# Kernel optimization log

Hardware: AMD Instinct MI355X
Metric: run time of the kernel (lower is better)

Reference implementation:

```python
import jax, jax.numpy as jnp
import numpy as np

B, T, CH, Hs, Ws = 2, 64, 512, 24, 24
DIM = CH // 2          # 256, attention channel dim
HEADS = 8
HEAD_DIM = DIM // HEADS  # 32
MAX_SEQ = 64


def setup_inputs() -> dict:
    key = jax.random.key(0)
    ks = jax.random.split(key, 6)
    return {
        "x": jax.random.normal(ks[0], (B, T, CH, Hs, Ws), dtype=jnp.float32),
        "rpb_table": jax.random.normal(ks[1], (2 * MAX_SEQ - 1, HEADS), dtype=jnp.float32) * 0.02,
        "qkv_w": jax.random.normal(ks[2], (3 * DIM, DIM), dtype=jnp.float32) * 0.02,
        "qkv_b": jax.random.normal(ks[3], (3 * DIM,), dtype=jnp.float32) * 0.02,
        "proj_w": jax.random.normal(ks[4], (DIM, DIM), dtype=jnp.float32) * 0.02,
        "proj_b": jax.random.normal(ks[5], (DIM,), dtype=jnp.float32) * 0.02,
    }


def reference(x, rpb_table, qkv_w, qkv_b, proj_w, proj_b):
    b, t, c, h, w = x.shape
    half = c // 2
    a_part = x[:, :, :half]       # (B,T,half,H,W) untouched branch
    b_part = x[:, :, half:]       # attention branch

    # 'b t c h w -> (b h w) t c'
    xb = jnp.transpose(b_part, (0, 3, 4, 1, 2)).reshape(b * h * w, t, half)
    B_, N, C = xb.shape
    scale = HEAD_DIM ** -0.5

    qkv = xb @ qkv_w.T + qkv_b                        # (B_, N, 3*C)
    qkv = qkv.reshape(B_, N, 3, HEADS, HEAD_DIM)
    qkv = jnp.transpose(qkv, (2, 0, 3, 1, 4))          # (3, B_, heads, N, hd)
    q, k, v = qkv[0] * scale, qkv[1], qkv[2]

    attn = jnp.einsum('bhnd,bhmd->bhnm', q, k)         # (B_, heads, N, N)

    # relative position bias: index = p2 - p1 + (MAX_SEQ - 1)
    pos = jnp.arange(t)
    rel_idx = pos[None, :] - pos[:, None] + (MAX_SEQ - 1)   # (N, N)
    bias = rpb_table[rel_idx]                              # (N, N, heads)
    bias = jnp.transpose(bias, (2, 0, 1))                  # (heads, N, N)
    attn = attn + bias[None]

    # causal (mask_future=True): -inf strictly above the diagonal
    causal = jnp.where(pos[None, :] > pos[:, None], -jnp.inf, 0.0).astype(attn.dtype)
    attn = attn + causal[None, None]

    attn = jax.nn.softmax(attn, axis=-1)

    out = jnp.einsum('bhnm,bhmd->bhnd', attn, v)       # (B_, heads, N, hd)
    out = jnp.transpose(out, (0, 2, 1, 3)).reshape(B_, N, C)
    out = out @ proj_w.T + proj_b

    # '(b h w) t c -> b t c h w'
    out = out.reshape(b, h, w, t, half)
    out = jnp.transpose(out, (0, 3, 4, 1, 2))

    return jnp.concatenate([a_part, out], axis=2)
```

## Files before the change

kernel.cpp:

```cpp
#include <hip/hip_runtime.h>
#include <hip/hip_bf16.h>

typedef __attribute__((ext_vector_type(4))) float  f32x4;
typedef __attribute__((ext_vector_type(8))) short  bf16x8;
typedef __attribute__((ext_vector_type(8))) unsigned short u16x8;
typedef __attribute__((ext_vector_type(4))) unsigned short u16x4;
typedef __attribute__((ext_vector_type(4))) int i32x4;

__device__ __forceinline__ unsigned short f2bf(float f) {
    union { float f; unsigned u; } v; v.f = f;
    unsigned u = v.u;
    unsigned r = u + 0x7fffu + ((u >> 16) & 1u);
    return (unsigned short)(r >> 16);
}

__device__ __forceinline__ unsigned cvtpk(float lo, float hi) {
    unsigned r;
    asm("v_cvt_pk_bf16_f32 %0, %1, %2" : "=v"(r) : "v"(lo), "v"(hi));
    return r;
}

__device__ __forceinline__ int selshfl(unsigned lo, unsigned hiw, int srcLane, bool hi) {
    int a = __shfl((int)lo, srcLane, 64);
    int b = __shfl((int)hiw, srcLane, 64);
    return hi ? b : a;
}

__device__ __forceinline__ bf16x8 mkfrag(int w0, int w1, int w2, int w3) {
    i32x4 t; t[0] = w0; t[1] = w1; t[2] = w2; t[3] = w3;
    return __builtin_bit_cast(bf16x8, t);
}

__device__ __forceinline__ void gload16(const void* g, void* l) {
    __builtin_amdgcn_global_load_lds((const __attribute__((address_space(1))) unsigned*)g,
                                     (__attribute__((address_space(3))) unsigned*)l, 16, 0, 0);
}

#define MFMA(A, B, C) __builtin_amdgcn_mfma_f32_16x16x32_bf16((A), (B), (C), 0, 0, 0)


__global__ void cvt_weights(const float* __restrict__ qkv_w, const float* __restrict__ proj_w,
                            unsigned short* __restrict__ wq, unsigned short* __restrict__ wp) {
    int i = blockIdx.x * 256 + threadIdx.x;
    if (i < 196608) wq[i] = f2bf(qkv_w[i]);
    else            wp[i - 196608] = f2bf(proj_w[i - 196608]);
}

__global__ __launch_bounds__(256) void transpose_b(const float* __restrict__ x,
                                                   unsigned short* __restrict__ xb,
                                                   float* __restrict__ outp) {
    __shared__ unsigned short tile[256][72];
    const int bt  = blockIdx.x;
    const int hw0 = blockIdx.y * 64;
    const int tid = threadIdx.x;
    {
        const size_t slab = (size_t)bt * 294912;
        #pragma unroll
        for (int it = 0; it < 16; ++it) {
            int idx = it * 256 + tid;
            int ch  = idx >> 4;
            int off = (idx & 15) * 4;
            size_t o = slab + (size_t)ch * 576 + hw0 + off;
            *(float4*)(outp + o) = *(const float4*)(x + o);
        }
    }
    const float* src = x + ((size_t)bt * 512 + 256) * 576 + hw0;
    const int c_sub = tid >> 4, l16 = tid & 15;
    #pragma unroll
    for (int it = 0; it < 16; ++it) {
        int cc = it * 16 + c_sub;
        const float4 v = *(const float4*)(src + (size_t)cc * 576 + l16 * 4);
        tile[cc][l16 * 4 + 0] = f2bf(v.x);
        tile[cc][l16 * 4 + 1] = f2bf(v.y);
        tile[cc][l16 * 4 + 2] = f2bf(v.z);
        tile[cc][l16 * 4 + 3] = f2bf(v.w);
    }
    __syncthreads();
    const int row = tid >> 2;
    const int cs  = (tid & 3) * 64;
    const int b = bt >> 6, t = bt & 63;
    size_t m = ((size_t)(b * 576 + hw0 + row)) * 64 + t;
    unsigned short* dst = xb + m * 256 + cs;
    #pragma unroll
    for (int q = 0; q < 8; ++q) {
        u16x8 v;
        #pragma unroll
        for (int u = 0; u < 8; ++u) v[u] = tile[cs + q * 8 + u][row];
        *(u16x8*)(dst + q * 8) = v;
    }
}

#define PKPAIR(D, A, B4) \
    const unsigned D##_0 = cvtpk(A[0] + B4.x, A[1] + B4.y); \
    const unsigned D##_1 = cvtpk(A[2] + B4.z, A[3] + B4.w);

#define MKF(DST, LO, HI_) \
    DST = mkfrag(selshfl(LO##_0, HI_##_0, lA, hi), selshfl(LO##_1, HI_##_1, lA, hi), \
                 selshfl(LO##_0, HI_##_0, lB, hi), selshfl(LO##_1, HI_##_1, lB, hi));

#define SM1(SC, JT, R) { \
    const int j_ = (JT) * 16 + 4 * g + (R); \
    int d_ = j_ - i_ + 63; d_ = d_ > 63 ? 63 : d_; \
    const float v_ = SC[R] * scale + bias_w[d_]; \
    const float e_ = (j_ > i_) ? 0.f : __expf(v_); \
    SC[R] = e_; rs += e_; }

#define SMROW(SC, JT) SM1(SC, JT, 0) SM1(SC, JT, 1) SM1(SC, JT, 2) SM1(SC, JT, 3)

#define ATT_COL(IT, QF, O0V, O1V) { \
    f32x4 Sc0{0.f,0.f,0.f,0.f}, Sc1{0.f,0.f,0.f,0.f}, Sc2{0.f,0.f,0.f,0.f}, Sc3{0.f,0.f,0.f,0.f}; \
    __builtin_amdgcn_s_setprio(1); \
    Sc0 = MFMA(kf0, QF, Sc0); Sc1 = MFMA(kf1, QF, Sc1); \
    Sc2 = MFMA(kf2, QF, Sc2); Sc3 = MFMA(kf3, QF, Sc3); \
    __builtin_amdgcn_s_setprio(0); \
    const int i_ = (IT) * 16 + c; \
    float rs = 0.f; \
    SMROW(Sc0, 0) SMROW(Sc1, 1) SMROW(Sc2, 2) SMROW(Sc3, 3) \
    rs += __shfl_xor(rs, 16, 64); \
    rs += __shfl_xor(rs, 32, 64); \
    const float inv = 1.0f / rs; \
    const unsigned p00 = cvtpk(Sc0[0]*inv, Sc0[1]*inv), p01 = cvtpk(Sc0[2]*inv, Sc0[3]*inv); \
    const unsigned p10 = cvtpk(Sc1[0]*inv, Sc1[1]*inv), p11 = cvtpk(Sc1[2]*inv, Sc1[3]*inv); \
    const unsigned p20 = cvtpk(Sc2[0]*inv, Sc2[1]*inv), p21 = cvtpk(Sc2[2]*inv, Sc2[3]*inv); \
    const unsigned p30 = cvtpk(Sc3[0]*inv, Sc3[1]*inv), p31 = cvtpk(Sc3[2]*inv, Sc3[3]*inv); \
    const bf16x8 pf0 = mkfrag(selshfl(p00, p10, lA, hi), selshfl(p01, p11, lA, hi), \
                              selshfl(p00, p10, lB, hi), selshfl(p01, p11, lB, hi)); \
    const bf16x8 pf1 = mkfrag(selshfl(p20, p30, lA, hi), selshfl(p21, p31, lA, hi), \
                              selshfl(p20, p30, lB, hi), selshfl(p21, p31, lB, hi)); \
    __builtin_amdgcn_s_setprio(1); \
    O0V = MFMA(vf00, pf0, O0V); O1V = MFMA(vf10, pf0, O1V); \
    O0V = MFMA(vf01, pf1, O0V); O1V = MFMA(vf11, pf1, O1V); \
    __builtin_amdgcn_s_setprio(0); }

#define OSTORE(OV, DT, IT) { \
    const int t_ = (IT) * 16 + c; \
    const int unit_ = w * 4 + (DT) * 2 + (g >> 1); \
    u16x4 v_; v_[0] = f2bf(OV[0]); v_[1] = f2bf(OV[1]); v_[2] = f2bf(OV[2]); v_[3] = f2bf(OV[3]); \
    *(u16x4*)(&xs[t_ * 256 + ((unit_ ^ (t_ & 7)) << 3) + 4 * (g & 1)]) = v_; }

__global__ __launch_bounds__(512, 4)
void fused_block(
    const unsigned short* __restrict__ xb,
    const unsigned short* __restrict__ wqkv,
    const unsigned short* __restrict__ wproj,
    const float* __restrict__ qkv_b,
    const float* __restrict__ proj_b,
    const float* __restrict__ rpb,
    float* __restrict__ out)
{
    __shared__ unsigned short xs[16384];
    __shared__ unsigned short VtAll[256 * 88];
    __shared__ float bias_s[8][64];

    const int tid  = threadIdx.x;
    const int lane = tid & 63, w = tid >> 6;
    const int c = lane & 15, g = lane >> 4;
    const int c7 = c & 7;
    const bool hi = g >= 2;
    const int lA = c + 16 * ((2 * g) & 3);
    const int lB = c + 16 * ((2 * g + 1) & 3);
    const int bid = blockIdx.x;
    const int p  = (bid & 7) * 144 + (bid >> 3);
    const int b  = p / 576, hw = p % 576;

    const unsigned short* src = xb + (size_t)p * 16384;
    #pragma unroll
    for (int it = 0; it < 4; ++it) {
        int U = it * 512 + tid;
        int r = U >> 5, u = U & 31;
        gload16(src + r * 256 + ((u ^ (r & 7)) << 3), &xs[U << 3]);
    }
    bias_s[tid & 7][tid >> 3] = rpb[tid];
    __syncthreads();

    const float* bias_w = bias_s[w];
    const float scale = 0.17677669529663687f;

    {
        f32x4 acc[2][4] = {};
        #pragma unroll
        for (int ks = 0; ks < 8; ++ks) {
            bf16x8 bx[4], af[2];
            #pragma unroll
            for (int b2 = 0; b2 < 4; ++b2)
                bx[b2] = *(const bf16x8*)(&xs[(b2 * 16 + c) * 256 + (((ks * 4 + g) ^ c7) << 3)]);
            #pragma unroll
            for (int a2 = 0; a2 < 2; ++a2)
                af[a2] = *(const bf16x8*)(wqkv + (size_t)(512 + w * 32 + a2 * 16 + c) * 256 + ks * 32 + g * 8);
            #pragma unroll
            for (int a2 = 0; a2 < 2; ++a2)
                #pragma unroll
                for (int b2 = 0; b2 < 4; ++b2)
                    acc[a2][b2] = MFMA(af[a2], bx[b2], acc[a2][b2]);
        }
        #pragma unroll
        for (int a2 = 0; a2 < 2; ++a2) {
            float4 bv = *(const float4*)(qkv_b + 512 + w * 32 + a2 * 16 + g * 4);
            #pragma unroll
            for (int b2 = 0; b2 < 4; ++b2) {
                int t = b2 * 16 + c;
                VtAll[(w * 32 + a2 * 16 + g * 4 + 0) * 88 + t] = f2bf(acc[a2][b2][0] + bv.x);
                VtAll[(w * 32 + a2 * 16 + g * 4 + 1) * 88 + t] = f2bf(acc[a2][b2][1] + bv.y);
                VtAll[(w * 32 + a2 * 16 + g * 4 + 2) * 88 + t] = f2bf(acc[a2][b2][2] + bv.z);
                VtAll[(w * 32 + a2 * 16 + g * 4 + 3) * 88 + t] = f2bf(acc[a2][b2][3] + bv.w);
            }
        }
    }

    bf16x8 kf0, kf1, kf2, kf3, qf0, qf1, qf2, qf3;
    {
        f32x4 ak[2][4] = {}, aq[2][4] = {};
        #pragma unroll
        for (int ks = 0; ks < 8; ++ks) {
            bf16x8 bx[4], afk[2], afq[2];
            #pragma unroll
            for (int b2 = 0; b2 < 4; ++b2)
                bx[b2] = *(const bf16x8*)(&xs[(b2 * 16 + c) * 256 + (((ks * 4 + g) ^ c7) << 3)]);
            #pragma unroll
            for (int a2 = 0; a2 < 2; ++a2) {
                afk[a2] = *(const bf16x8*)(wqkv + (size_t)(256 + w * 32 + a2 * 16 + c) * 256 + ks * 32 + g * 8);
                afq[a2] = *(const bf16x8*)(wqkv + (size_t)(      w * 32 + a2 * 16 + c) * 256 + ks * 32 + g * 8);
            }
            #pragma unroll
            for (int a2 = 0; a2 < 2; ++a2)
                #pragma unroll
                for (int b2 = 0; b2 < 4; ++b2) {
                    ak[a2][b2] = MFMA(afk[a2], bx[b2], ak[a2][b2]);
                    aq[a2][b2] = MFMA(afq[a2], bx[b2], aq[a2][b2]);
                }
        }
        const float4 bk0 = *(const float4*)(qkv_b + 256 + w * 32 + g * 4);
        const float4 bk1 = *(const float4*)(qkv_b + 256 + w * 32 + 16 + g * 4);
        const float4 bq0 = *(const float4*)(qkv_b +       w * 32 + g * 4);
        const float4 bq1 = *(const float4*)(qkv_b +       w * 32 + 16 + g * 4);
        PKPAIR(kp00, ak[0][0], bk0) PKPAIR(kp01, ak[0][1], bk0)
        PKPAIR(kp02, ak[0][2], bk0) PKPAIR(kp03, ak[0][3], bk0)
        PKPAIR(kp10, ak[1][0], bk1) PKPAIR(kp11, ak[1][1], bk1)
        PKPAIR(kp12, ak[1][2], bk1) PKPAIR(kp13, ak[1][3], bk1)
        PKPAIR(qp00, aq[0][0], bq0) PKPAIR(qp01, aq[0][1], bq0)
        PKPAIR(qp02, aq[0][2], bq0) PKPAIR(qp03, aq[0][3], bq0)
        PKPAIR(qp10, aq[1][0], bq1) PKPAIR(qp11, aq[1][1], bq1)
        PKPAIR(qp12, aq[1][2], bq1) PKPAIR(qp13, aq[1][3], bq1)
        MKF(kf0, kp00, kp10) MKF(kf1, kp01, kp11) MKF(kf2, kp02, kp12) MKF(kf3, kp03, kp13)
        MKF(qf0, qp00, qp10) MKF(qf1, qp01, qp11) MKF(qf2, qp02, qp12) MKF(qf3, qp03, qp13)
    }

    const bf16x8 vf00 = *(const bf16x8*)(&VtAll[(w * 32 +  0 + c) * 88 +  0 + g * 8]);
    const bf16x8 vf01 = *(const bf16x8*)(&VtAll[(w * 32 +  0 + c) * 88 + 32 + g * 8]);
    const bf16x8 vf10 = *(const bf16x8*)(&VtAll[(w * 32 + 16 + c) * 88 +  0 + g * 8]);
    const bf16x8 vf11 = *(const bf16x8*)(&VtAll[(w * 32 + 16 + c) * 88 + 32 + g * 8]);

    f32x4 O00{0.f,0.f,0.f,0.f}, O01{0.f,0.f,0.f,0.f}, O02{0.f,0.f,0.f,0.f}, O03{0.f,0.f,0.f,0.f};
    f32x4 O10{0.f,0.f,0.f,0.f}, O11{0.f,0.f,0.f,0.f}, O12{0.f,0.f,0.f,0.f}, O13{0.f,0.f,0.f,0.f};
    ATT_COL(0, qf0, O00, O10)
    ATT_COL(1, qf1, O01, O11)
    ATT_COL(2, qf2, O02, O12)
    ATT_COL(3, qf3, O03, O13)

    __syncthreads();
    OSTORE(O00, 0, 0) OSTORE(O01, 0, 1) OSTORE(O02, 0, 2) OSTORE(O03, 0, 3)
    OSTORE(O10, 1, 0) OSTORE(O11, 1, 1) OSTORE(O12, 1, 2) OSTORE(O13, 1, 3)
    __syncthreads();

    f32x4 ap[2][4] = {};
    #pragma unroll
    for (int ks = 0; ks < 8; ++ks) {
        bf16x8 af[2], bx[4];
        #pragma unroll
        for (int a2 = 0; a2 < 2; ++a2)
            af[a2] = *(const bf16x8*)(wproj + (size_t)(w * 32 + a2 * 16 + c) * 256 + ks * 32 + g * 8);
        #pragma unroll
        for (int b2 = 0; b2 < 4; ++b2)
            bx[b2] = *(const bf16x8*)(&xs[(b2 * 16 + c) * 256 + (((ks * 4 + g) ^ c7) << 3)]);
        #pragma unroll
        for (int a2 = 0; a2 < 2; ++a2)
            #pragma unroll
            for (int b2 = 0; b2 < 4; ++b2)
                ap[a2][b2] = MFMA(af[a2], bx[b2], ap[a2][b2]);
    }
    #pragma unroll
    for (int a2 = 0; a2 < 2; ++a2) {
        int n = w * 32 + a2 * 16 + g * 4;
        float4 pb = *(const float4*)(proj_b + n);
        #pragma unroll
        for (int b2 = 0; b2 < 4; ++b2) {
            int t = b2 * 16 + c;
            float* dst = out + ((size_t)((b * 64 + t) * 512 + 256 + n)) * 576 + hw;
            dst[0]        = ap[a2][b2][0] + pb.x;
            dst[576]      = ap[a2][b2][1] + pb.y;
            dst[2 * 576]  = ap[a2][b2][2] + pb.z;
            dst[3 * 576]  = ap[a2][b2][3] + pb.w;
        }
    }
}

extern "C" void kernel_launch(void* const* d_in, const int* in_sizes, int n_in,
                              void* d_out, int out_size, void* d_ws, size_t ws_size,
                              hipStream_t stream) {
    (void)in_sizes; (void)n_in; (void)out_size;
    const float* x      = (const float*)d_in[0];
    const float* rpb    = (const float*)d_in[1];
    const float* qkv_w  = (const float*)d_in[2];
    const float* qkv_b  = (const float*)d_in[3];
    const float* proj_w = (const float*)d_in[4];
    const float* proj_b = (const float*)d_in[5];
    float* out = (float*)d_out;

    char* ws = (char*)d_ws;
    unsigned short* wq = (unsigned short*)ws;
    unsigned short* wp = (unsigned short*)(ws + 393216);
    unsigned short* xb = (unsigned short*)(ws + 524288);
    if (ws_size < (size_t)524288 + 37748736) return;

    cvt_weights<<<1024, 256, 0, stream>>>(qkv_w, proj_w, wq, wp);
    transpose_b<<<dim3(128, 9), 256, 0, stream>>>(x, xb, out);
    fused_block<<<1152, 512, 0, stream>>>(xb, wq, wp, qkv_b, proj_b, rpb, out);
}
```

Measured before the change: 247.4 us.

## Split fused block into per-head attention kernel plus separate tiled projection GEMM

Replaces the single fused kernel, which handled one spatial position with 512 threads, with two kernels. The first is a per-head attention kernel with one wave per (position, head): it computes Q, K and V by reading x directly from global memory, then writes the bf16 attention output to a new workspace buffer. The second is a separate 128x128 tiled GEMM for the output projection, with LDS staging and swizzling. The aim is to raise occupancy and parallelism and to make the projection GEMM more efficient. The cost is an extra round trip through global memory for the intermediate of about 37MB, plus an additional kernel launch; the setprio hints are also removed.

```diff
diff --git a/kernel.cpp b/kernel.cpp
--- a/kernel.cpp
+++ b/kernel.cpp
@@ -109,10 +109,8 @@
 
 #define ATT_COL(IT, QF, O0V, O1V) { \
     f32x4 Sc0{0.f,0.f,0.f,0.f}, Sc1{0.f,0.f,0.f,0.f}, Sc2{0.f,0.f,0.f,0.f}, Sc3{0.f,0.f,0.f,0.f}; \
-    __builtin_amdgcn_s_setprio(1); \
     Sc0 = MFMA(kf0, QF, Sc0); Sc1 = MFMA(kf1, QF, Sc1); \
     Sc2 = MFMA(kf2, QF, Sc2); Sc3 = MFMA(kf3, QF, Sc3); \
-    __builtin_amdgcn_s_setprio(0); \
     const int i_ = (IT) * 16 + c; \
     float rs = 0.f; \
     SMROW(Sc0, 0) SMROW(Sc1, 1) SMROW(Sc2, 2) SMROW(Sc3, 3) \
@@ -127,112 +125,85 @@
                               selshfl(p00, p10, lB, hi), selshfl(p01, p11, lB, hi)); \
     const bf16x8 pf1 = mkfrag(selshfl(p20, p30, lA, hi), selshfl(p21, p31, lA, hi), \
                               selshfl(p20, p30, lB, hi), selshfl(p21, p31, lB, hi)); \
-    __builtin_amdgcn_s_setprio(1); \
     O0V = MFMA(vf00, pf0, O0V); O1V = MFMA(vf10, pf0, O1V); \
-    O0V = MFMA(vf01, pf1, O0V); O1V = MFMA(vf11, pf1, O1V); \
-    __builtin_amdgcn_s_setprio(0); }
-
-#define OSTORE(OV, DT, IT) { \
+    O0V = MFMA(vf01, pf1, O0V); O1V = MFMA(vf11, pf1, O1V); }
+
+#define OSTOREG(OV, DT, IT) { \
     const int t_ = (IT) * 16 + c; \
-    const int unit_ = w * 4 + (DT) * 2 + (g >> 1); \
     u16x4 v_; v_[0] = f2bf(OV[0]); v_[1] = f2bf(OV[1]); v_[2] = f2bf(OV[2]); v_[3] = f2bf(OV[3]); \
-    *(u16x4*)(&xs[t_ * 256 + ((unit_ ^ (t_ & 7)) << 3) + 4 * (g & 1)]) = v_; }
-
-__global__ __launch_bounds__(512, 4)
-void fused_block(
+    *(u16x4*)(att + ((size_t)(t_ * 1152 + p)) * 256 + h * 32 + (DT) * 16 + 4 * g) = v_; }
+
+__global__ __launch_bounds__(256, 3)
+void attn_heads(
     const unsigned short* __restrict__ xb,
     const unsigned short* __restrict__ wqkv,
-    const unsigned short* __restrict__ wproj,
     const float* __restrict__ qkv_b,
-    const float* __restrict__ proj_b,
     const float* __restrict__ rpb,
-    float* __restrict__ out)
+    unsigned short* __restrict__ att)
 {
-    __shared__ unsigned short xs[16384];
-    __shared__ unsigned short VtAll[256 * 88];
+    __shared__ unsigned short vt[4][32 * 88];
     __shared__ float bias_s[8][64];
 
     const int tid  = threadIdx.x;
     const int lane = tid & 63, w = tid >> 6;
     const int c = lane & 15, g = lane >> 4;
-    const int c7 = c & 7;
     const bool hi = g >= 2;
     const int lA = c + 16 * ((2 * g) & 3);
     const int lB = c + 16 * ((2 * g + 1) & 3);
-    const int bid = blockIdx.x;
-    const int p  = (bid & 7) * 144 + (bid >> 3);
-    const int b  = p / 576, hw = p % 576;
-
-    const unsigned short* src = xb + (size_t)p * 16384;
-    #pragma unroll
-    for (int it = 0; it < 4; ++it) {
-        int U = it * 512 + tid;
-        int r = U >> 5, u = U & 31;
-        gload16(src + r * 256 + ((u ^ (r & 7)) << 3), &xs[U << 3]);
-    }
+
     bias_s[tid & 7][tid >> 3] = rpb[tid];
+    bias_s[(tid + 256) & 7][(tid + 256) >> 3] = rpb[tid + 256];
     __syncthreads();
 
-    const float* bias_w = bias_s[w];
+    const int gw = blockIdx.x * 4 + w;
+    const int h  = gw / 1152;
+    const int p  = gw - h * 1152;
+    const float* bias_w = bias_s[h];
     const float scale = 0.17677669529663687f;
-
-    {
-        f32x4 acc[2][4] = {};
-        #pragma unroll
-        for (int ks = 0; ks < 8; ++ks) {
-            bf16x8 bx[4], af[2];
-            #pragma unroll
-            for (int b2 = 0; b2 < 4; ++b2)
-                bx[b2] = *(const bf16x8*)(&xs[(b2 * 16 + c) * 256 + (((ks * 4 + g) ^ c7) << 3)]);
-            #pragma unroll
-            for (int a2 = 0; a2 < 2; ++a2)
-                af[a2] = *(const bf16x8*)(wqkv + (size_t)(512 + w * 32 + a2 * 16 + c) * 256 + ks * 32 + g * 8);
-            #pragma unroll
-            for (int a2 = 0; a2 < 2; ++a2)
-                #pragma unroll
-                for (int b2 = 0; b2 < 4; ++b2)
-                    acc[a2][b2] = MFMA(af[a2], bx[b2], acc[a2][b2]);
-        }
+    const unsigned short* xrow = xb + (size_t)p * 16384;
+    unsigned short* vts = vt[w];
+
+    f32x4 aq[2][4] = {}, ak[2][4] = {}, av[2][4] = {};
+    #pragma unroll
+    for (int ks = 0; ks < 8; ++ks) {
+        bf16x8 bx[4];
+        #pragma unroll
+        for (int b2 = 0; b2 < 4; ++b2)
+            bx[b2] = *(const bf16x8*)(xrow + (b2 * 16 + c) * 256 + ks * 32 + g * 8);
         #pragma unroll
         for (int a2 = 0; a2 < 2; ++a2) {
-            float4 bv = *(const float4*)(qkv_b + 512 + w * 32 + a2 * 16 + g * 4);
+            const size_t ko = (size_t)ks * 32 + g * 8;
+            const bf16x8 fq = *(const bf16x8*)(wqkv + (size_t)(      h * 32 + a2 * 16 + c) * 256 + ko);
+            const bf16x8 fk = *(const bf16x8*)(wqkv + (size_t)(256 + h * 32 + a2 * 16 + c) * 256 + ko);
+            const bf16x8 fv = *(const bf16x8*)(wqkv + (size_t)(512 + h * 32 + a2 * 16 + c) * 256 + ko);
             #pragma unroll
             for (int b2 = 0; b2 < 4; ++b2) {
-                int t = b2 * 16 + c;
-                VtAll[(w * 32 + a2 * 16 + g * 4 + 0) * 88 + t] = f2bf(acc[a2][b2][0] + bv.x);
-                VtAll[(w * 32 + a2 * 16 + g * 4 + 1) * 88 + t] = f2bf(acc[a2][b2][1] + bv.y);
-                VtAll[(w * 32 + a2 * 16 + g * 4 + 2) * 88 + t] = f2bf(acc[a2][b2][2] + bv.z);
-                VtAll[(w * 32 + a2 * 16 + g * 4 + 3) * 88 + t] = f2bf(acc[a2][b2][3] + bv.w);
+                aq[a2][b2] = MFMA(fq, bx[b2], aq[a2][b2]);
+                ak[a2][b2] = MFMA(fk, bx[b2], ak[a2][b2]);
+                av[a2][b2] = MFMA(fv, bx[b2], av[a2][b2]);
             }
+        }
+    }
+
+    #pragma unroll
+    for (int a2 = 0; a2 < 2; ++a2) {
+        float4 bv = *(const float4*)(qkv_b + 512 + h * 32 + a2 * 16 + g * 4);
+        #pragma unroll
+        for (int b2 = 0; b2 < 4; ++b2) {
+            int t = b2 * 16 + c;
+            vts[(a2 * 16 + g * 4 + 0) * 88 + t] = f2bf(av[a2][b2][0] + bv.x);
+            vts[(a2 * 16 + g * 4 + 1) * 88 + t] = f2bf(av[a2][b2][1] + bv.y);
+            vts[(a2 * 16 + g * 4 + 2) * 88 + t] = f2bf(av[a2][b2][2] + bv.z);
+            vts[(a2 * 16 + g * 4 + 3) * 88 + t] = f2bf(av[a2][b2][3] + bv.w);
         }
     }
 
     bf16x8 kf0, kf1, kf2, kf3, qf0, qf1, qf2, qf3;
     {
-        f32x4 ak[2][4] = {}, aq[2][4] = {};
-        #pragma unroll
-        for (int ks = 0; ks < 8; ++ks) {
-            bf16x8 bx[4], afk[2], afq[2];
-            #pragma unroll
-            for (int b2 = 0; b2 < 4; ++b2)
-                bx[b2] = *(const bf16x8*)(&xs[(b2 * 16 + c) * 256 + (((ks * 4 + g) ^ c7) << 3)]);
-            #pragma unroll
-            for (int a2 = 0; a2 < 2; ++a2) {
-                afk[a2] = *(const bf16x8*)(wqkv + (size_t)(256 + w * 32 + a2 * 16 + c) * 256 + ks * 32 + g * 8);
-                afq[a2] = *(const bf16x8*)(wqkv + (size_t)(      w * 32 + a2 * 16 + c) * 256 + ks * 32 + g * 8);
-            }
-            #pragma unroll
-            for (int a2 = 0; a2 < 2; ++a2)
-                #pragma unroll
-                for (int b2 = 0; b2 < 4; ++b2) {
-                    ak[a2][b2] = MFMA(afk[a2], bx[b2], ak[a2][b2]);
-                    aq[a2][b2] = MFMA(afq[a2], bx[b2], aq[a2][b2]);
-                }
-        }
-        const float4 bk0 = *(const float4*)(qkv_b + 256 + w * 32 + g * 4);
-        const float4 bk1 = *(const float4*)(qkv_b + 256 + w * 32 + 16 + g * 4);
-        const float4 bq0 = *(const float4*)(qkv_b +       w * 32 + g * 4);
-        const float4 bq1 = *(const float4*)(qkv_b +       w * 32 + 16 + g * 4);
+        const float4 bk0 = *(const float4*)(qkv_b + 256 + h * 32 + g * 4);
+        const float4 bk1 = *(const float4*)(qkv_b + 256 + h * 32 + 16 + g * 4);
+        const float4 bq0 = *(const float4*)(qkv_b +       h * 32 + g * 4);
+        const float4 bq1 = *(const float4*)(qkv_b +       h * 32 + 16 + g * 4);
         PKPAIR(kp00, ak[0][0], bk0) PKPAIR(kp01, ak[0][1], bk0)
         PKPAIR(kp02, ak[0][2], bk0) PKPAIR(kp03, ak[0][3], bk0)
         PKPAIR(kp10, ak[1][0], bk1) PKPAIR(kp11, ak[1][1], bk1)
@@ -245,10 +216,10 @@
         MKF(qf0, qp00, qp10) MKF(qf1, qp01, qp11) MKF(qf2, qp02, qp12) MKF(qf3, qp03, qp13)
     }
 
-    const bf16x8 vf00 = *(const bf16x8*)(&VtAll[(w * 32 +  0 + c) * 88 +  0 + g * 8]);
-    const bf16x8 vf01 = *(const bf16x8*)(&VtAll[(w * 32 +  0 + c) * 88 + 32 + g * 8]);
-    const bf16x8 vf10 = *(const bf16x8*)(&VtAll[(w * 32 + 16 + c) * 88 +  0 + g * 8]);
-    const bf16x8 vf11 = *(const bf16x8*)(&VtAll[(w * 32 + 16 + c) * 88 + 32 + g * 8]);
+    const bf16x8 vf00 = *(const bf16x8*)(&vts[( 0 + c) * 88 +  0 + g * 8]);
+    const bf16x8 vf01 = *(const bf16x8*)(&vts[( 0 + c) * 88 + 32 + g * 8]);
+    const bf16x8 vf10 = *(const bf16x8*)(&vts[(16 + c) * 88 +  0 + g * 8]);
+    const bf16x8 vf11 = *(const bf16x8*)(&vts[(16 + c) * 88 + 32 + g * 8]);
 
     f32x4 O00{0.f,0.f,0.f,0.f}, O01{0.f,0.f,0.f,0.f}, O02{0.f,0.f,0.f,0.f}, O03{0.f,0.f,0.f,0.f};
     f32x4 O10{0.f,0.f,0.f,0.f}, O11{0.f,0.f,0.f,0.f}, O12{0.f,0.f,0.f,0.f}, O13{0.f,0.f,0.f,0.f};
@@ -257,39 +228,66 @@
     ATT_COL(2, qf2, O02, O12)
     ATT_COL(3, qf3, O03, O13)
 
-    __syncthreads();
-    OSTORE(O00, 0, 0) OSTORE(O01, 0, 1) OSTORE(O02, 0, 2) OSTORE(O03, 0, 3)
-    OSTORE(O10, 1, 0) OSTORE(O11, 1, 1) OSTORE(O12, 1, 2) OSTORE(O13, 1, 3)
-    __syncthreads();
-
-    f32x4 ap[2][4] = {};
-    #pragma unroll
-    for (int ks = 0; ks < 8; ++ks) {
-        bf16x8 af[2], bx[4];
-        #pragma unroll
-        for (int a2 = 0; a2 < 2; ++a2)
-            af[a2] = *(const bf16x8*)(wproj + (size_t)(w * 32 + a2 * 16 + c) * 256 + ks * 32 + g * 8);
-        #pragma unroll
-        for (int b2 = 0; b2 < 4; ++b2)
-            bx[b2] = *(const bf16x8*)(&xs[(b2 * 16 + c) * 256 + (((ks * 4 + g) ^ c7) << 3)]);
-        #pragma unroll
-        for (int a2 = 0; a2 < 2; ++a2)
+    OSTOREG(O00, 0, 0) OSTOREG(O01, 0, 1) OSTOREG(O02, 0, 2) OSTOREG(O03, 0, 3)
+    OSTOREG(O10, 1, 0) OSTOREG(O11, 1, 1) OSTOREG(O12, 1, 2) OSTOREG(O13, 1, 3)
+}
+
+__global__ __launch_bounds__(256, 4) void gemm_proj(const unsigned short* __restrict__ A,
+                                                    const unsigned short* __restrict__ Wt,
+                                                    const float* __restrict__ bias,
+                                                    float* __restrict__ out) {
+    __shared__ unsigned short Ws[128 * 64];
+    __shared__ unsigned short Xs[128 * 64];
+    const int m0 = blockIdx.x * 128, n0 = blockIdx.y * 128;
+    const int tid = threadIdx.x;
+    const int lane = tid & 63, w = tid >> 6;
+    const int wy = w >> 1, wx = w & 1;
+    const int c = lane & 15, g = lane >> 4;
+    const int lr = lane >> 3, lu = lane & 7;
+    const int su = lu ^ lr;
+    const int cs7 = c & 7;
+    f32x4 acc[4][4] = {};
+    for (int k0 = 0; k0 < 256; k0 += 64) {
+        #pragma unroll
+        for (int q = 0; q < 4; ++q) {
+            int R = w * 32 + q * 8;
+            gload16(Wt + (size_t)(n0 + R + lr) * 256 + k0 + su * 8, &Ws[R * 64]);
+            gload16(A  + (size_t)(m0 + R + lr) * 256 + k0 + su * 8, &Xs[R * 64]);
+        }
+        __syncthreads();
+        #pragma unroll
+        for (int kk = 0; kk < 2; ++kk) {
+            bf16x8 af[4], bx[4];
+            #pragma unroll
+            for (int a2 = 0; a2 < 4; ++a2)
+                af[a2] = *(const bf16x8*)(&Ws[(wy * 64 + a2 * 16 + c) * 64 + (((kk * 4 + g) ^ cs7) * 8)]);
             #pragma unroll
             for (int b2 = 0; b2 < 4; ++b2)
-                ap[a2][b2] = MFMA(af[a2], bx[b2], ap[a2][b2]);
-    }
-    #pragma unroll
-    for (int a2 = 0; a2 < 2; ++a2) {
-        int n = w * 32 + a2 * 16 + g * 4;
-        float4 pb = *(const float4*)(proj_b + n);
+                bx[b2] = *(const bf16x8*)(&Xs[(wx * 64 + b2 * 16 + c) * 64 + (((kk * 4 + g) ^ cs7) * 8)]);
+            #pragma unroll
+            for (int a2 = 0; a2 < 4; ++a2)
+                #pragma unroll
+                for (int b2 = 0; b2 < 4; ++b2)
+                    acc[a2][b2] = MFMA(af[a2], bx[b2], acc[a2][b2]);
+        }
+        __syncthreads();
+    }
+    #pragma unroll
+    for (int a2 = 0; a2 < 4; ++a2) {
+        int n = n0 + wy * 64 + a2 * 16 + g * 4;
+        float4 bv = *(const float4*)(bias + n);
         #pragma unroll
         for (int b2 = 0; b2 < 4; ++b2) {
-            int t = b2 * 16 + c;
-            float* dst = out + ((size_t)((b * 64 + t) * 512 + 256 + n)) * 576 + hw;
-            dst[0]        = ap[a2][b2][0] + pb.x;
-            dst[576]      = ap[a2][b2][1] + pb.y;
-            dst[2 * 576]  = ap[a2][b2][2] + pb.z;
-            dst[3 * 576]  = ap[a2][b2][3] + pb.w;
+            int m = m0 + wx * 64 + b2 * 16 + c;
+            int t   = m / 1152;
+            int rem = m % 1152;
+            int bb  = rem / 576;
+            int hw  = rem % 576;
+            float* dst = out + ((size_t)(bb * 64 + t) * 512 + 256 + n) * 576 + hw;
+            dst[0]        = acc[a2][b2][0] + bv.x;
+            dst[576]      = acc[a2][b2][1] + bv.y;
+            dst[2 * 576]  = acc[a2][b2][2] + bv.z;
+            dst[3 * 576]  = acc[a2][b2][3] + bv.w;
         }
     }
 }
@@ -307,12 +305,14 @@
     float* out = (float*)d_out;
 
     char* ws = (char*)d_ws;
-    unsigned short* wq = (unsigned short*)ws;
-    unsigned short* wp = (unsigned short*)(ws + 393216);
-    unsigned short* xb = (unsigned short*)(ws + 524288);
-    if (ws_size < (size_t)524288 + 37748736) return;
+    unsigned short* wq  = (unsigned short*)ws;
+    unsigned short* wp  = (unsigned short*)(ws + 393216);
+    unsigned short* xb  = (unsigned short*)(ws + 524288);
+    unsigned short* att = (unsigned short*)(ws + 524288 + 37748736);
+    if (ws_size < (size_t)524288 + 2 * 37748736) return;
 
     cvt_weights<<<1024, 256, 0, stream>>>(qkv_w, proj_w, wq, wp);
     transpose_b<<<dim3(128, 9), 256, 0, stream>>>(x, xb, out);
-    fused_block<<<1152, 512, 0, stream>>>(xb, wq, wp, qkv_b, proj_b, rpb, out);
-}
+    attn_heads<<<2304, 256, 0, stream>>>(xb, wq, qkv_b, rpb, att);
+    gemm_proj<<<dim3(576, 2), 256, 0, stream>>>(att, wp, proj_b, out);
+}
```

Result: faster. 227.5 us (-8.1%).

## Read activations directly from global and merge QKV GEMMs into one pass

Applied to the files above, without the earlier changes.

The x tile is no longer staged into LDS with global_load_lds. Each wave reads its B fragments straight from global memory, and the Q, K and V projections are computed in a single k-loop that reuses each activation fragment across three weight sets. V^T and the attention output now share one smaller LDS region, which lowers LDS use per block and should allow more occupancy. The setprio hints around the MFMAs are removed. Every wave now reloads the same 32 KB activation tile from global or L2, which replaces cheap LDS reads with uncoalesced global reads. The fused loop also holds more accumulators live, raising register pressure.

```diff
diff --git a/kernel.cpp b/kernel.cpp
--- a/kernel.cpp
+++ b/kernel.cpp
@@ -29,11 +29,6 @@
 __device__ __forceinline__ bf16x8 mkfrag(int w0, int w1, int w2, int w3) {
     i32x4 t; t[0] = w0; t[1] = w1; t[2] = w2; t[3] = w3;
     return __builtin_bit_cast(bf16x8, t);
-}
-
-__device__ __forceinline__ void gload16(const void* g, void* l) {
-    __builtin_amdgcn_global_load_lds((const __attribute__((address_space(1))) unsigned*)g,
-                                     (__attribute__((address_space(3))) unsigned*)l, 16, 0, 0);
 }
 
 #define MFMA(A, B, C) __builtin_amdgcn_mfma_f32_16x16x32_bf16((A), (B), (C), 0, 0, 0)
@@ -109,10 +104,8 @@
 
 #define ATT_COL(IT, QF, O0V, O1V) { \
     f32x4 Sc0{0.f,0.f,0.f,0.f}, Sc1{0.f,0.f,0.f,0.f}, Sc2{0.f,0.f,0.f,0.f}, Sc3{0.f,0.f,0.f,0.f}; \
-    __builtin_amdgcn_s_setprio(1); \
     Sc0 = MFMA(kf0, QF, Sc0); Sc1 = MFMA(kf1, QF, Sc1); \
     Sc2 = MFMA(kf2, QF, Sc2); Sc3 = MFMA(kf3, QF, Sc3); \
-    __builtin_amdgcn_s_setprio(0); \
     const int i_ = (IT) * 16 + c; \
     float rs = 0.f; \
     SMROW(Sc0, 0) SMROW(Sc1, 1) SMROW(Sc2, 2) SMROW(Sc3, 3) \
@@ -127,19 +120,17 @@
                               selshfl(p00, p10, lB, hi), selshfl(p01, p11, lB, hi)); \
     const bf16x8 pf1 = mkfrag(selshfl(p20, p30, lA, hi), selshfl(p21, p31, lA, hi), \
                               selshfl(p20, p30, lB, hi), selshfl(p21, p31, lB, hi)); \
-    __builtin_amdgcn_s_setprio(1); \
     O0V = MFMA(vf00, pf0, O0V); O1V = MFMA(vf10, pf0, O1V); \
-    O0V = MFMA(vf01, pf1, O0V); O1V = MFMA(vf11, pf1, O1V); \
-    __builtin_amdgcn_s_setprio(0); }
+    O0V = MFMA(vf01, pf1, O0V); O1V = MFMA(vf11, pf1, O1V); }
 
 #define OSTORE(OV, DT, IT) { \
     const int t_ = (IT) * 16 + c; \
     const int unit_ = w * 4 + (DT) * 2 + (g >> 1); \
     u16x4 v_; v_[0] = f2bf(OV[0]); v_[1] = f2bf(OV[1]); v_[2] = f2bf(OV[2]); v_[3] = f2bf(OV[3]); \
-    *(u16x4*)(&xs[t_ * 256 + ((unit_ ^ (t_ & 7)) << 3) + 4 * (g & 1)]) = v_; }
+    *(u16x4*)(&att_s[t_ * 256 + ((unit_ ^ (t_ & 7)) << 3) + 4 * (g & 1)]) = v_; }
 
 __global__ __launch_bounds__(512, 4)
-void fused_block(
+void fused_attn_proj(
     const unsigned short* __restrict__ xb,
     const unsigned short* __restrict__ wqkv,
     const unsigned short* __restrict__ wproj,
@@ -148,8 +139,7 @@
     const float* __restrict__ rpb,
     float* __restrict__ out)
 {
-    __shared__ unsigned short xs[16384];
-    __shared__ unsigned short VtAll[256 * 88];
+    __shared__ unsigned short region[18432];
     __shared__ float bias_s[8][64];
 
     const int tid  = threadIdx.x;
@@ -159,80 +149,61 @@
     const bool hi = g >= 2;
     const int lA = c + 16 * ((2 * g) & 3);
     const int lB = c + 16 * ((2 * g + 1) & 3);
+
+    bias_s[tid & 7][tid >> 3] = rpb[tid];
+    __syncthreads();
+
+    const int h  = w;
     const int bid = blockIdx.x;
     const int p  = (bid & 7) * 144 + (bid >> 3);
     const int b  = p / 576, hw = p % 576;
-
-    const unsigned short* src = xb + (size_t)p * 16384;
-    #pragma unroll
-    for (int it = 0; it < 4; ++it) {
-        int U = it * 512 + tid;
-        int r = U >> 5, u = U & 31;
-        gload16(src + r * 256 + ((u ^ (r & 7)) << 3), &xs[U << 3]);
-    }
-    bias_s[tid & 7][tid >> 3] = rpb[tid];
-    __syncthreads();
-
-    const float* bias_w = bias_s[w];
+    const float* bias_w = bias_s[h];
     const float scale = 0.17677669529663687f;
-
-    {
-        f32x4 acc[2][4] = {};
-        #pragma unroll
-        for (int ks = 0; ks < 8; ++ks) {
-            bf16x8 bx[4], af[2];
-            #pragma unroll
-            for (int b2 = 0; b2 < 4; ++b2)
-                bx[b2] = *(const bf16x8*)(&xs[(b2 * 16 + c) * 256 + (((ks * 4 + g) ^ c7) << 3)]);
-            #pragma unroll
-            for (int a2 = 0; a2 < 2; ++a2)
-                af[a2] = *(const bf16x8*)(wqkv + (size_t)(512 + w * 32 + a2 * 16 + c) * 256 + ks * 32 + g * 8);
-            #pragma unroll
-            for (int a2 = 0; a2 < 2; ++a2)
-                #pragma unroll
-                for (int b2 = 0; b2 < 4; ++b2)
-                    acc[a2][b2] = MFMA(af[a2], bx[b2], acc[a2][b2]);
-        }
+    const unsigned short* xrow = xb + (size_t)p * 16384;
+    unsigned short* vts   = region + w * 2304;
+    unsigned short* att_s = region;
+
+    f32x4 aq[2][4] = {}, ak[2][4] = {}, av[2][4] = {};
+    #pragma unroll
+    for (int ks = 0; ks < 8; ++ks) {
+        bf16x8 bx[4];
+        #pragma unroll
+        for (int b2 = 0; b2 < 4; ++b2)
+            bx[b2] = *(const bf16x8*)(xrow + (b2 * 16 + c) * 256 + ks * 32 + g * 8);
         #pragma unroll
         for (int a2 = 0; a2 < 2; ++a2) {
-            float4 bv = *(const float4*)(qkv_b + 512 + w * 32 + a2 * 16 + g * 4);
+            const size_t ko = (size_t)ks * 32 + g * 8;
+            const bf16x8 fq = *(const bf16x8*)(wqkv + (size_t)(      h * 32 + a2 * 16 + c) * 256 + ko);
+            const bf16x8 fk = *(const bf16x8*)(wqkv + (size_t)(256 + h * 32 + a2 * 16 + c) * 256 + ko);
+            const bf16x8 fv = *(const bf16x8*)(wqkv + (size_t)(512 + h * 32 + a2 * 16 + c) * 256 + ko);
             #pragma unroll
             for (int b2 = 0; b2 < 4; ++b2) {
-                int t = b2 * 16 + c;
-                VtAll[(w * 32 + a2 * 16 + g * 4 + 0) * 88 + t] = f2bf(acc[a2][b2][0] + bv.x);
-                VtAll[(w * 32 + a2 * 16 + g * 4 + 1) * 88 + t] = f2bf(acc[a2][b2][1] + bv.y);
-                VtAll[(w * 32 + a2 * 16 + g * 4 + 2) * 88 + t] = f2bf(acc[a2][b2][2] + bv.z);
-                VtAll[(w * 32 + a2 * 16 + g * 4 + 3) * 88 + t] = f2bf(acc[a2][b2][3] + bv.w);
+                aq[a2][b2] = MFMA(fq, bx[b2], aq[a2][b2]);
+                ak[a2][b2] = MFMA(fk, bx[b2], ak[a2][b2]);
+                av[a2][b2] = MFMA(fv, bx[b2], av[a2][b2]);
             }
+        }
+    }
+
+    #pragma unroll
+    for (int a2 = 0; a2 < 2; ++a2) {
+        float4 bv = *(const float4*)(qkv_b + 512 + h * 32 + a2 * 16 + g * 4);
+        #pragma unroll
+        for (int b2 = 0; b2 < 4; ++b2) {
+            int t = b2 * 16 + c;
+            vts[(a2 * 16 + g * 4 + 0) * 72 + t] = f2bf(av[a2][b2][0] + bv.x);
+            vts[(a2 * 16 + g * 4 + 1) * 72 + t] = f2bf(av[a2][b2][1] + bv.y);
+            vts[(a2 * 16 + g * 4 + 2) * 72 + t] = f2bf(av[a2][b2][2] + bv.z);
+            vts[(a2 * 16 + g * 4 + 3) * 72 + t] = f2bf(av[a2][b2][3] + bv.w);
         }
     }
 
     bf16x8 kf0, kf1, kf2, kf3, qf0, qf1, qf2, qf3;
     {
-        f32x4 ak[2][4] = {}, aq[2][4] = {};
-        #pragma unroll
-        for (int ks = 0; ks < 8; ++ks) {
-            bf16x8 bx[4], afk[2], afq[2];
-            #pragma unroll
-            for (int b2 = 0; b2 < 4; ++b2)
-                bx[b2] = *(const bf16x8*)(&xs[(b2 * 16 + c) * 256 + (((ks * 4 + g) ^ c7) << 3)]);
-            #pragma unroll
-            for (int a2 = 0; a2 < 2; ++a2) {
-                afk[a2] = *(const bf16x8*)(wqkv + (size_t)(256 + w * 32 + a2 * 16 + c) * 256 + ks * 32 + g * 8);
-                afq[a2] = *(const bf16x8*)(wqkv + (size_t)(      w * 32 + a2 * 16 + c) * 256 + ks * 32 + g * 8);
-            }
-            #pragma unroll
-            for (int a2 = 0; a2 < 2; ++a2)
-                #pragma unroll
-                for (int b2 = 0; b2 < 4; ++b2) {
-                    ak[a2][b2] = MFMA(afk[a2], bx[b2], ak[a2][b2]);
-                    aq[a2][b2] = MFMA(afq[a2], bx[b2], aq[a2][b2]);
-                }
-        }
-        const float4 bk0 = *(const float4*)(qkv_b + 256 + w * 32 + g * 4);
-        const float4 bk1 = *(const float4*)(qkv_b + 256 + w * 32 + 16 + g * 4);
-        const float4 bq0 = *(const float4*)(qkv_b +       w * 32 + g * 4);
-        const float4 bq1 = *(const float4*)(qkv_b +       w * 32 + 16 + g * 4);
+        const float4 bk0 = *(const float4*)(qkv_b + 256 + h * 32 + g * 4);
+        const float4 bk1 = *(const float4*)(qkv_b + 256 + h * 32 + 16 + g * 4);
+        const float4 bq0 = *(const float4*)(qkv_b +       h * 32 + g * 4);
+        const float4 bq1 = *(const float4*)(qkv_b +       h * 32 + 16 + g * 4);
         PKPAIR(kp00, ak[0][0], bk0) PKPAIR(kp01, ak[0][1], bk0)
         PKPAIR(kp02, ak[0][2], bk0) PKPAIR(kp03, ak[0][3], bk0)
         PKPAIR(kp10, ak[1][0], bk1) PKPAIR(kp11, ak[1][1], bk1)
@@ -245,10 +216,12 @@
         MKF(qf0, qp00, qp10) MKF(qf1, qp01, qp11) MKF(qf2, qp02, qp12) MKF(qf3, qp03, qp13)
     }
 
-    const bf16x8 vf00 = *(const bf16x8*)(&VtAll[(w * 32 +  0 + c) * 88 +  0 + g * 8]);
-    const bf16x8 vf01 = *(const bf16x8*)(&VtAll[(w * 32 +  0 + c) * 88 + 32 + g * 8]);
-    const bf16x8 vf10 = *(const bf16x8*)(&VtAll[(w * 32 + 16 + c) * 88 +  0 + g * 8]);
-    const bf16x8 vf11 = *(const bf16x8*)(&VtAll[(w * 32 + 16 + c) * 88 + 32 + g * 8]);
+    const bf16x8 vf00 = *(const bf16x8*)(&vts[( 0 + c) * 72 +  0 + g * 8]);
+    const bf16x8 vf01 = *(const bf16x8*)(&vts[( 0 + c) * 72 + 32 + g * 8]);
+    const bf16x8 vf10 = *(const bf16x8*)(&vts[(16 + c) * 72 +  0 + g * 8]);
+    const bf16x8 vf11 = *(const bf16x8*)(&vts[(16 + c) * 72 + 32 + g * 8]);
+
+    __syncthreads();
 
     f32x4 O00{0.f,0.f,0.f,0.f}, O01{0.f,0.f,0.f,0.f}, O02{0.f,0.f,0.f,0.f}, O03{0.f,0.f,0.f,0.f};
     f32x4 O10{0.f,0.f,0.f,0.f}, O11{0.f,0.f,0.f,0.f}, O12{0.f,0.f,0.f,0.f}, O13{0.f,0.f,0.f,0.f};
@@ -257,9 +230,10 @@
     ATT_COL(2, qf2, O02, O12)
     ATT_COL(3, qf3, O03, O13)
 
-    __syncthreads();
-    OSTORE(O00, 0, 0) OSTORE(O01, 0, 1) OSTORE(O02, 0, 2) OSTORE(O03, 0, 3)
-    OSTORE(O10, 1, 0) OSTORE(O11, 1, 1) OSTORE(O12, 1, 2) OSTORE(O13, 1, 3)
+    OSTORE(O00, 0, 0) OSTORE(O10, 1, 0)
+    OSTORE(O01, 0, 1) OSTORE(O11, 1, 1)
+    OSTORE(O02, 0, 2) OSTORE(O12, 1, 2)
+    OSTORE(O03, 0, 3) OSTORE(O13, 1, 3)
     __syncthreads();
 
     f32x4 ap[2][4] = {};
@@ -271,7 +245,7 @@
             af[a2] = *(const bf16x8*)(wproj + (size_t)(w * 32 + a2 * 16 + c) * 256 + ks * 32 + g * 8);
         #pragma unroll
         for (int b2 = 0; b2 < 4; ++b2)
-            bx[b2] = *(const bf16x8*)(&xs[(b2 * 16 + c) * 256 + (((ks * 4 + g) ^ c7) << 3)]);
+            bx[b2] = *(const bf16x8*)(&att_s[(b2 * 16 + c) * 256 + (((ks * 4 + g) ^ c7) << 3)]);
         #pragma unroll
         for (int a2 = 0; a2 < 2; ++a2)
             #pragma unroll
@@ -314,5 +288,5 @@
 
     cvt_weights<<<1024, 256, 0, stream>>>(qkv_w, proj_w, wq, wp);
     transpose_b<<<dim3(128, 9), 256, 0, stream>>>(x, xb, out);
-    fused_block<<<1152, 512, 0, stream>>>(xb, wq, wp, qkv_b, proj_b, rpb, out);
-}
+    fused_attn_proj<<<1152, 512, 0, stream>>>(xb, wq, wp, qkv_b, proj_b, rpb, out);
+}
```

Result: slower. 383.6 us (+55.0%).
